# Kernel tuning notes

Hardware: AMD Instinct MI355X
Metric: run time of the kernel (lower is better)

Reference implementation:

```python
import jax, jax.numpy as jnp
import numpy as np

N_NODES = 50000
N_EDGES = 800000
IN_DIM = 128
HID = 128
OUT_DIM = 128
N_LAYERS = 6
NUM_GRAPHS = 128


def setup_inputs() -> dict:
    key = jax.random.key(0)
    ks = jax.random.split(key, 16)
    s = 0.05
    inp = {
        "x": jax.random.normal(ks[0], (N_NODES, IN_DIM), jnp.float32),
        "edge_index": jax.random.randint(ks[1], (2, N_EDGES), 0, N_NODES, jnp.int64 if jax.config.jax_enable_x64 else jnp.int32).astype(jnp.int32),
        "batch": jnp.sort(jax.random.randint(ks[2], (N_NODES,), 0, NUM_GRAPHS).astype(jnp.int32)),
        # pre linear
        "pre_w": jax.random.normal(ks[3], (IN_DIM, HID), jnp.float32) * s,
        "pre_b": jnp.zeros((HID,), jnp.float32),
        # GIN mlp per layer: Linear(H,H) -> ReLU -> Linear(H,H)
        "conv_w1": jax.random.normal(ks[4], (N_LAYERS, HID, HID), jnp.float32) * s,
        "conv_b1": jnp.zeros((N_LAYERS, HID), jnp.float32),
        "conv_w2": jax.random.normal(ks[5], (N_LAYERS, HID, HID), jnp.float32) * s,
        "conv_b2": jnp.zeros((N_LAYERS, HID), jnp.float32),
        # post MLP: Linear(7H, H) -> ReLU -> Linear(H, out)
        "post_w1": jax.random.normal(ks[6], (HID * (N_LAYERS + 1), HID), jnp.float32) * s,
        "post_b1": jnp.zeros((HID,), jnp.float32),
        "post_w2": jax.random.normal(ks[7], (HID, OUT_DIM), jnp.float32) * s,
        "post_b2": jnp.zeros((OUT_DIM,), jnp.float32),
    }
    return inp


def reference(x, edge_index, batch, pre_w, pre_b, conv_w1, conv_b1, conv_w2, conv_b2,
              post_w1, post_b1, post_w2, post_b2):
    src, dst = edge_index[0], edge_index[1]
    # pre linear
    h = x @ pre_w + pre_b  # [N, H]
    emb_list = [h]
    xres = h
    for i in range(N_LAYERS):
        # GINConv (eps=0): agg_j x_j over in-edges, then (1+eps)*x + agg -> MLP
        msg = h[src]  # [E, H] gather
        agg = jax.ops.segment_sum(msg, dst, num_segments=N_NODES)  # scatter-add
        z = h + agg
        z = jax.nn.relu(z @ conv_w1[i] + conv_b1[i]) @ conv_w2[i] + conv_b2[i]
        if i & 1:
            z = z + xres
            xres = z
        h = jax.nn.relu(z)
        emb_list.append(h)
    emb = jnp.concatenate(emb_list, axis=1)  # [N, (L+1)*H]
    # global add pool over graphs
    pooled = jax.ops.segment_sum(emb, batch, num_segments=NUM_GRAPHS)  # [G, (L+1)*H]
    out = jax.nn.relu(pooled @ post_w1 + post_b1) @ post_w2 + post_b2  # [G, OUT]
    return out
```

## Files before the change

kernel.cpp:

```cpp
#include <hip/hip_runtime.h>
#include <hip/hip_bf16.h>

#define HID 128

using bf16x8 = __attribute__((ext_vector_type(8))) short;
using f32x4  = __attribute__((ext_vector_type(4))) float;

__device__ inline float bf2f(unsigned int u16) {
    union { float f; unsigned int i; } v; v.i = u16 << 16; return v.f;
}
__device__ inline unsigned short f2bf(float f) {
    __hip_bfloat16 h = __float2bfloat16(f);
    return *reinterpret_cast<unsigned short*>(&h);
}


__global__ void zero_i32(int* __restrict__ p, int n) {
    int i = blockIdx.x * blockDim.x + threadIdx.x;
    if (i < n) p[i] = 0;
}

__global__ void count_deg(const int* __restrict__ dst, int* __restrict__ deg, int E) {
    int e = blockIdx.x * blockDim.x + threadIdx.x;
    if (e < E) atomicAdd(&deg[dst[e]], 1);
}

__global__ __launch_bounds__(256) void block_sums(const int* __restrict__ deg,
                                                  int* __restrict__ bsum, int n) {
    __shared__ int red[256];
    int t = threadIdx.x;
    int i = blockIdx.x * 256 + t;
    red[t] = (i < n) ? deg[i] : 0;
    __syncthreads();
    for (int off = 128; off > 0; off >>= 1) {
        if (t < off) red[t] += red[t + off];
        __syncthreads();
    }
    if (t == 0) bsum[blockIdx.x] = red[0];
}

__global__ __launch_bounds__(1024) void scan_bsums(const int* __restrict__ bsum,
                                                   int* __restrict__ bstart, int nb) {
    __shared__ int s[1024];
    int t = threadIdx.x;
    s[t] = (t < nb) ? bsum[t] : 0;
    __syncthreads();
    for (int off = 1; off < 1024; off <<= 1) {
        int v = (t >= off) ? s[t - off] : 0;
        __syncthreads();
        s[t] += v;
        __syncthreads();
    }
    if (t < nb) bstart[t] = (t == 0) ? 0 : s[t - 1];
}

__global__ __launch_bounds__(256) void scan_within(const int* __restrict__ deg,
                                                   const int* __restrict__ bstart,
                                                   int* __restrict__ row_ptr,
                                                   int* __restrict__ pos, int n) {
    __shared__ int s[256];
    int b = blockIdx.x, t = threadIdx.x;
    int i = b * 256 + t;
    int v = (i < n) ? deg[i] : 0;
    s[t] = v;
    __syncthreads();
    for (int off = 1; off < 256; off <<= 1) {
        int u = (t >= off) ? s[t - off] : 0;
        __syncthreads();
        s[t] += u;
        __syncthreads();
    }
    if (i < n) {
        int excl = bstart[b] + s[t] - v;
        row_ptr[i] = excl;
        pos[i] = excl;
        if (i == n - 1) row_ptr[n] = bstart[b] + s[t];
    }
}

__global__ void fill_csr(const int* __restrict__ src, const int* __restrict__ dst,
                         int* __restrict__ pos, int* __restrict__ csr_src, int E) {
    int e = blockIdx.x * blockDim.x + threadIdx.x;
    if (e < E) {
        int p = atomicAdd(&pos[dst[e]], 1);
        csr_src[p] = src[e];
    }
}

__global__ void graph_starts(const int* __restrict__ batch, int* __restrict__ gstart,
                             int n, int G) {
    int g = blockIdx.x * blockDim.x + threadIdx.x;
    if (g > G) return;
    int lo = 0, hi = n;
    while (lo < hi) { int m = (lo + hi) >> 1; if (batch[m] < g) lo = m + 1; else hi = m; }
    gstart[g] = lo;
}


__global__ void f32_to_bf16_vec(const float* __restrict__ in,
                                unsigned short* __restrict__ out, int n8) {
    int i = blockIdx.x * blockDim.x + threadIdx.x;
    if (i >= n8) return;
    const float4* in4 = (const float4*)in;
    float4 a = in4[i * 2], b = in4[i * 2 + 1];
    uint4 o;
    o.x = f2bf(a.x) | ((unsigned)f2bf(a.y) << 16);
    o.y = f2bf(a.z) | ((unsigned)f2bf(a.w) << 16);
    o.z = f2bf(b.x) | ((unsigned)f2bf(b.y) << 16);
    o.w = f2bf(b.z) | ((unsigned)f2bf(b.w) << 16);
    ((uint4*)out)[i] = o;
}

__global__ void transpose_kc(const float* __restrict__ W, unsigned short* __restrict__ Wt,
                             int K, int C, int total) {
    int tid = blockIdx.x * blockDim.x + threadIdx.x;
    if (tid >= total) return;
    int kc = K * C;
    int mat = tid / kc;
    int rem = tid - mat * kc;
    int c = rem / K;
    int k = rem - c * K;
    Wt[tid] = f2bf(W[(size_t)mat * kc + (size_t)k * C + c]);
}

template <bool ODD>
__global__ __launch_bounds__(128) void fused_layer(const unsigned short* __restrict__ emb,
                                                   int slice_u4, int row_u4,
                                                   const int* __restrict__ row_ptr,
                                                   const int* __restrict__ csr_src,
                                                   const unsigned short* __restrict__ Wt1,
                                                   const float* __restrict__ b1,
                                                   const unsigned short* __restrict__ Wt2,
                                                   const float* __restrict__ b2,
                                                   unsigned short* __restrict__ xres,
                                                   unsigned short* __restrict__ h_out,
                                                   int out_stride, int N) {
    __shared__ __align__(16) char zt[16 * 256];
    __shared__ __align__(16) char tt[16 * 256];
    int t = threadIdx.x;
    int rowbase = blockIdx.x * 16;

    {
        int nl = t >> 3;
        int lane8 = t & 7;
        int node = rowbase + nl;
        const uint4* h4 = (const uint4*)emb;
        float sa0=0,sa1=0,sa2=0,sa3=0,sa4=0,sa5=0,sa6=0,sa7=0;
        float sb0=0,sb1=0,sb2=0,sb3=0,sb4=0,sb5=0,sb6=0,sb7=0;
        if (node < N) {
            size_t base = (size_t)node * row_u4 + slice_u4;
            uint4 u0 = h4[base + lane8];
            uint4 u1 = h4[base + lane8 + 8];
            sa0 = bf2f(u0.x & 0xffff); sa1 = bf2f(u0.x >> 16);
            sa2 = bf2f(u0.y & 0xffff); sa3 = bf2f(u0.y >> 16);
            sa4 = bf2f(u0.z & 0xffff); sa5 = bf2f(u0.z >> 16);
            sa6 = bf2f(u0.w & 0xffff); sa7 = bf2f(u0.w >> 16);
            sb0 = bf2f(u1.x & 0xffff); sb1 = bf2f(u1.x >> 16);
            sb2 = bf2f(u1.y & 0xffff); sb3 = bf2f(u1.y >> 16);
            sb4 = bf2f(u1.z & 0xffff); sb5 = bf2f(u1.z >> 16);
            sb6 = bf2f(u1.w & 0xffff); sb7 = bf2f(u1.w >> 16);
            int e0 = row_ptr[node], e1 = row_ptr[node + 1];
            int e = e0;
            for (; e + 1 < e1; e += 2) {
                int n0 = csr_src[e], n1 = csr_src[e + 1];
                size_t p0 = (size_t)n0 * row_u4 + slice_u4;
                size_t p1 = (size_t)n1 * row_u4 + slice_u4;
                uint4 v0 = h4[p0 + lane8];
                uint4 v1 = h4[p0 + lane8 + 8];
                uint4 w0 = h4[p1 + lane8];
                uint4 w1 = h4[p1 + lane8 + 8];
                sa0 += bf2f(v0.x & 0xffff); sa1 += bf2f(v0.x >> 16);
                sa2 += bf2f(v0.y & 0xffff); sa3 += bf2f(v0.y >> 16);
                sa4 += bf2f(v0.z & 0xffff); sa5 += bf2f(v0.z >> 16);
                sa6 += bf2f(v0.w & 0xffff); sa7 += bf2f(v0.w >> 16);
                sb0 += bf2f(v1.x & 0xffff); sb1 += bf2f(v1.x >> 16);
                sb2 += bf2f(v1.y & 0xffff); sb3 += bf2f(v1.y >> 16);
                sb4 += bf2f(v1.z & 0xffff); sb5 += bf2f(v1.z >> 16);
                sb6 += bf2f(v1.w & 0xffff); sb7 += bf2f(v1.w >> 16);
                sa0 += bf2f(w0.x & 0xffff); sa1 += bf2f(w0.x >> 16);
                sa2 += bf2f(w0.y & 0xffff); sa3 += bf2f(w0.y >> 16);
                sa4 += bf2f(w0.z & 0xffff); sa5 += bf2f(w0.z >> 16);
                sa6 += bf2f(w0.w & 0xffff); sa7 += bf2f(w0.w >> 16);
                sb0 += bf2f(w1.x & 0xffff); sb1 += bf2f(w1.x >> 16);
                sb2 += bf2f(w1.y & 0xffff); sb3 += bf2f(w1.y >> 16);
                sb4 += bf2f(w1.z & 0xffff); sb5 += bf2f(w1.z >> 16);
                sb6 += bf2f(w1.w & 0xffff); sb7 += bf2f(w1.w >> 16);
            }
            if (e < e1) {
                size_t p0 = (size_t)csr_src[e] * row_u4 + slice_u4;
                uint4 v0 = h4[p0 + lane8];
                uint4 v1 = h4[p0 + lane8 + 8];
                sa0 += bf2f(v0.x & 0xffff); sa1 += bf2f(v0.x >> 16);
                sa2 += bf2f(v0.y & 0xffff); sa3 += bf2f(v0.y >> 16);
                sa4 += bf2f(v0.z & 0xffff); sa5 += bf2f(v0.z >> 16);
                sa6 += bf2f(v0.w & 0xffff); sa7 += bf2f(v0.w >> 16);
                sb0 += bf2f(v1.x & 0xffff); sb1 += bf2f(v1.x >> 16);
                sb2 += bf2f(v1.y & 0xffff); sb3 += bf2f(v1.y >> 16);
                sb4 += bf2f(v1.z & 0xffff); sb5 += bf2f(v1.z >> 16);
                sb6 += bf2f(v1.w & 0xffff); sb7 += bf2f(v1.w >> 16);
            }
        }
        uint4 oa, ob;
        oa.x = f2bf(sa0) | ((unsigned)f2bf(sa1) << 16);
        oa.y = f2bf(sa2) | ((unsigned)f2bf(sa3) << 16);
        oa.z = f2bf(sa4) | ((unsigned)f2bf(sa5) << 16);
        oa.w = f2bf(sa6) | ((unsigned)f2bf(sa7) << 16);
        ob.x = f2bf(sb0) | ((unsigned)f2bf(sb1) << 16);
        ob.y = f2bf(sb2) | ((unsigned)f2bf(sb3) << 16);
        ob.z = f2bf(sb4) | ((unsigned)f2bf(sb5) << 16);
        ob.w = f2bf(sb6) | ((unsigned)f2bf(sb7) << 16);
        int swz = (nl & 7) << 4;
        *(uint4*)(zt + nl * 256 + ((lane8 * 16) ^ swz)) = oa;
        *(uint4*)(zt + nl * 256 + (((lane8 + 8) * 16) ^ swz)) = ob;
    }
    __syncthreads();

    int wave = t >> 6, lane = t & 63, l15 = lane & 15, l4 = lane >> 4;
    int colbase = wave * 64;

    f32x4 acc[4];
#pragma unroll
    for (int ct = 0; ct < 4; ct++) acc[ct] = (f32x4){0.f, 0.f, 0.f, 0.f};

#pragma unroll
    for (int kk = 0; kk < 4; kk++) {
        int k0 = kk * 32 + l4 * 8;
        bf16x8 a0 = *(const bf16x8*)(zt + l15 * 256 + ((k0 * 2) ^ ((l15 & 7) << 4)));
#pragma unroll
        for (int ct = 0; ct < 4; ct++) {
            bf16x8 b = *(const bf16x8*)&Wt1[(size_t)(colbase + ct * 16 + l15) * HID + k0];
            acc[ct] = __builtin_amdgcn_mfma_f32_16x16x32_bf16(a0, b, acc[ct], 0, 0, 0);
        }
    }

#pragma unroll
    for (int ct = 0; ct < 4; ct++) {
        int col = colbase + ct * 16 + l15;
        float bc = b1[col];
#pragma unroll
        for (int j = 0; j < 4; j++) {
            int r = l4 * 4 + j;
            float v = fmaxf(acc[ct][j] + bc, 0.f);
            *(unsigned short*)(tt + r * 256 + ((col * 2) ^ ((r & 7) << 4))) = f2bf(v);
        }
    }
    __syncthreads();

#pragma unroll
    for (int ct = 0; ct < 4; ct++) acc[ct] = (f32x4){0.f, 0.f, 0.f, 0.f};
#pragma unroll
    for (int kk = 0; kk < 4; kk++) {
        int k0 = kk * 32 + l4 * 8;
        bf16x8 a0 = *(const bf16x8*)(tt + l15 * 256 + ((k0 * 2) ^ ((l15 & 7) << 4)));
#pragma unroll
        for (int ct = 0; ct < 4; ct++) {
            bf16x8 b = *(const bf16x8*)&Wt2[(size_t)(colbase + ct * 16 + l15) * HID + k0];
            acc[ct] = __builtin_amdgcn_mfma_f32_16x16x32_bf16(a0, b, acc[ct], 0, 0, 0);
        }
    }

#pragma unroll
    for (int ct = 0; ct < 4; ct++) {
        int col = colbase + ct * 16 + l15;
        float bc = b2[col];
#pragma unroll
        for (int j = 0; j < 4; j++) {
            int r = l4 * 4 + j;
            int rg = rowbase + r;
            if (rg < N) {
                float v = acc[ct][j] + bc;
                if (ODD) {
                    v += bf2f(xres[(size_t)rg * HID + col]);
                    xres[(size_t)rg * HID + col] = f2bf(v);
                }
                h_out[(size_t)rg * out_stride + col] = f2bf(fmaxf(v, 0.f));
            }
        }
    }
}

__global__ __launch_bounds__(256) void linear_pre(const unsigned short* __restrict__ in,
                                                  const unsigned short* __restrict__ Wt,
                                                  const float* __restrict__ bias,
                                                  unsigned short* __restrict__ out,
                                                  int out_stride,
                                                  unsigned short* __restrict__ pre_out, int M) {
    int tid = threadIdx.x;
    int wave = tid >> 6, lane = tid & 63;
    int l15 = lane & 15, l4 = lane >> 4;
    int rowbase = blockIdx.x * 64 + wave * 16;
    f32x4 acc[8];
#pragma unroll
    for (int ct = 0; ct < 8; ct++) acc[ct] = (f32x4){0.f, 0.f, 0.f, 0.f};
    int r0 = min(rowbase + l15, M - 1);
#pragma unroll
    for (int kk = 0; kk < 4; kk++) {
        int k0 = kk * 32 + l4 * 8;
        bf16x8 a0 = *(const bf16x8*)&in[(size_t)r0 * HID + k0];
#pragma unroll
        for (int ct = 0; ct < 8; ct++) {
            bf16x8 b = *(const bf16x8*)&Wt[(size_t)(ct * 16 + l15) * HID + k0];
            acc[ct] = __builtin_amdgcn_mfma_f32_16x16x32_bf16(a0, b, acc[ct], 0, 0, 0);
        }
    }
#pragma unroll
    for (int ct = 0; ct < 8; ct++) {
        int col = ct * 16 + l15;
        float bc = bias[col];
#pragma unroll
        for (int j = 0; j < 4; j++) {
            int r = rowbase + l4 * 4 + j;
            if (r < M) {
                float v = acc[ct][j] + bc;
                unsigned short bv = f2bf(v);
                pre_out[(size_t)r * HID + col] = bv;
                out[(size_t)r * out_stride + col] = bv;
            }
        }
    }
}

__global__ __launch_bounds__(128) void pool_all(const unsigned short* __restrict__ emb,
                                                const int* __restrict__ gstart,
                                                float* __restrict__ part, int EMB) {
    int g = blockIdx.x >> 3, sub = blockIdx.x & 7;
    int t = threadIdx.x;
    if (t >= 112) return;
    const uint4* e4 = (const uint4*)emb;
    int row_u4 = EMB / 8;
    int n0 = gstart[g], n1 = gstart[g + 1];
    float s[8] = {0.f, 0.f, 0.f, 0.f, 0.f, 0.f, 0.f, 0.f};
    for (int n = n0 + sub; n < n1; n += 8) {
        uint4 v = e4[(size_t)n * row_u4 + t];
        s[0] += bf2f(v.x & 0xffff); s[1] += bf2f(v.x >> 16);
        s[2] += bf2f(v.y & 0xffff); s[3] += bf2f(v.y >> 16);
        s[4] += bf2f(v.z & 0xffff); s[5] += bf2f(v.z >> 16);
        s[6] += bf2f(v.w & 0xffff); s[7] += bf2f(v.w >> 16);
    }
    float4* p4 = (float4*)&part[(size_t)blockIdx.x * EMB + t * 8];
    p4[0] = (float4){s[0], s[1], s[2], s[3]};
    p4[1] = (float4){s[4], s[5], s[6], s[7]};
}

__global__ __launch_bounds__(128) void pool_fin(const float* __restrict__ part,
                                                unsigned short* __restrict__ pooled,
                                                int EMB) {
    int idx = blockIdx.x * 128 + threadIdx.x;
    int g = idx / EMB, c = idx - g * EMB;
    float s = 0.f;
#pragma unroll
    for (int sub = 0; sub < 8; sub++)
        s += part[(size_t)(g * 8 + sub) * EMB + c];
    pooled[idx] = f2bf(s);
}

__global__ __launch_bounds__(256) void post_mfma(const unsigned short* __restrict__ pooled,
                                                 const unsigned short* __restrict__ w1t,
                                                 const float* __restrict__ b1,
                                                 const unsigned short* __restrict__ w2t,
                                                 const float* __restrict__ b2,
                                                 float* __restrict__ out, int EMB) {
    __shared__ __align__(16) char lds[128 * 256];
    int t = threadIdx.x;
    int wave = t >> 6, lane = t & 63, l15 = lane & 15, l4 = lane >> 4;
    int wrow = wave * 32;
    f32x4 acc[2][8];
#pragma unroll
    for (int rt = 0; rt < 2; rt++)
#pragma unroll
        for (int ct = 0; ct < 8; ct++) acc[rt][ct] = (f32x4){0.f, 0.f, 0.f, 0.f};
    int r0 = wrow + l15, r1 = r0 + 16;
#pragma unroll 4
    for (int kk = 0; kk < EMB / 32; kk++) {
        int k0 = kk * 32 + l4 * 8;
        bf16x8 a0 = *(const bf16x8*)&pooled[(size_t)r0 * EMB + k0];
        bf16x8 a1 = *(const bf16x8*)&pooled[(size_t)r1 * EMB + k0];
#pragma unroll
        for (int ct = 0; ct < 8; ct++) {
            bf16x8 b = *(const bf16x8*)&w1t[(size_t)(ct * 16 + l15) * EMB + k0];
            acc[0][ct] = __builtin_amdgcn_mfma_f32_16x16x32_bf16(a0, b, acc[0][ct], 0, 0, 0);
            acc[1][ct] = __builtin_amdgcn_mfma_f32_16x16x32_bf16(a1, b, acc[1][ct], 0, 0, 0);
        }
    }
#pragma unroll
    for (int ct = 0; ct < 8; ct++) {
        int col = ct * 16 + l15;
        float bc = b1[col];
#pragma unroll
        for (int rt = 0; rt < 2; rt++)
#pragma unroll
            for (int j = 0; j < 4; j++) {
                int r = wrow + rt * 16 + l4 * 4 + j;
                float v = fmaxf(acc[rt][ct][j] + bc, 0.f);
                *(unsigned short*)(lds + r * 256 + ((col * 2) ^ ((r & 7) << 4))) = f2bf(v);
            }
    }
    __syncthreads();
#pragma unroll
    for (int rt = 0; rt < 2; rt++)
#pragma unroll
        for (int ct = 0; ct < 8; ct++) acc[rt][ct] = (f32x4){0.f, 0.f, 0.f, 0.f};
#pragma unroll
    for (int kk = 0; kk < 4; kk++) {
        int k0 = kk * 32 + l4 * 8;
        bf16x8 a0 = *(const bf16x8*)(lds + r0 * 256 + ((k0 * 2) ^ ((r0 & 7) << 4)));
        bf16x8 a1 = *(const bf16x8*)(lds + r1 * 256 + ((k0 * 2) ^ ((r1 & 7) << 4)));
#pragma unroll
        for (int ct = 0; ct < 8; ct++) {
            bf16x8 b = *(const bf16x8*)&w2t[(size_t)(ct * 16 + l15) * HID + k0];
            acc[0][ct] = __builtin_amdgcn_mfma_f32_16x16x32_bf16(a0, b, acc[0][ct], 0, 0, 0);
            acc[1][ct] = __builtin_amdgcn_mfma_f32_16x16x32_bf16(a1, b, acc[1][ct], 0, 0, 0);
        }
    }
#pragma unroll
    for (int ct = 0; ct < 8; ct++) {
        int col = ct * 16 + l15;
        float bc = b2[col];
#pragma unroll
        for (int rt = 0; rt < 2; rt++)
#pragma unroll
            for (int j = 0; j < 4; j++) {
                int r = wrow + rt * 16 + l4 * 4 + j;
                out[(size_t)r * HID + col] = acc[rt][ct][j] + bc;
            }
    }
}


extern "C" void kernel_launch(void* const* d_in, const int* in_sizes, int n_in,
                              void* d_out, int out_size, void* d_ws, size_t ws_size,
                              hipStream_t stream) {
    const float* x       = (const float*)d_in[0];
    const int* edge_index= (const int*)d_in[1];
    const int* batch     = (const int*)d_in[2];
    const float* pre_w   = (const float*)d_in[3];
    const float* pre_b   = (const float*)d_in[4];
    const float* conv_w1 = (const float*)d_in[5];
    const float* conv_b1 = (const float*)d_in[6];
    const float* conv_w2 = (const float*)d_in[7];
    const float* conv_b2 = (const float*)d_in[8];
    const float* post_w1 = (const float*)d_in[9];
    const float* post_b1 = (const float*)d_in[10];
    const float* post_w2 = (const float*)d_in[11];
    const float* post_b2 = (const float*)d_in[12];
    float* outp = (float*)d_out;

    int N = in_sizes[0] / HID;
    int E = in_sizes[1] / 2;
    int L = in_sizes[5] / (HID * HID);
    int G = out_size / HID;
    int EMB = (L + 1) * HID;

    const int* src = edge_index;
    const int* dst = edge_index + E;

    char* w = (char*)d_ws;
    auto alloc = [&](size_t bytes) -> char* {
        char* p = w;
        w += (bytes + 255) & ~(size_t)255;
        return p;
    };
    unsigned short* emb   = (unsigned short*)alloc((size_t)N * EMB * 2);
    unsigned short* x_bf  = (unsigned short*)alloc((size_t)N * HID * 2);
    unsigned short* xres  = (unsigned short*)alloc((size_t)N * HID * 2);
    float* part   = (float*)alloc((size_t)G * 8 * EMB * 4);
    unsigned short* pooled = (unsigned short*)alloc((size_t)G * EMB * 2);
    unsigned short* Wt_pre = (unsigned short*)alloc((size_t)HID * HID * 2);
    unsigned short* Wt_c1  = (unsigned short*)alloc((size_t)L * HID * HID * 2);
    unsigned short* Wt_c2  = (unsigned short*)alloc((size_t)L * HID * HID * 2);
    unsigned short* w1t    = (unsigned short*)alloc((size_t)EMB * HID * 2);
    unsigned short* w2t    = (unsigned short*)alloc((size_t)HID * HID * 2);
    int* deg      = (int*)alloc((size_t)(N + 1) * 4);
    int* row_ptr  = (int*)alloc((size_t)(N + 1) * 4);
    int* pos      = (int*)alloc((size_t)(N + 1) * 4);
    int* bsum     = (int*)alloc((size_t)1024 * 4);
    int* bstart   = (int*)alloc((size_t)1024 * 4);
    int* csr_src  = (int*)alloc((size_t)E * 4);
    int* gstart   = (int*)alloc((size_t)(G + 1) * 4);
    (void)ws_size; (void)n_in;

    int eb = (E + 255) / 256;
    int nb = (N + 255) / 256;

    zero_i32<<<nb, 256, 0, stream>>>(deg, N);
    count_deg<<<eb, 256, 0, stream>>>(dst, deg, E);
    block_sums<<<nb, 256, 0, stream>>>(deg, bsum, N);
    scan_bsums<<<1, 1024, 0, stream>>>(bsum, bstart, nb);
    scan_within<<<nb, 256, 0, stream>>>(deg, bstart, row_ptr, pos, N);
    fill_csr<<<eb, 256, 0, stream>>>(src, dst, pos, csr_src, E);
    graph_starts<<<1, 256, 0, stream>>>(batch, gstart, N, G);

    f32_to_bf16_vec<<<(N * HID / 8 + 255) / 256, 256, 0, stream>>>(x, x_bf, N * HID / 8);
    transpose_kc<<<(HID * HID + 255) / 256, 256, 0, stream>>>(pre_w, Wt_pre, HID, HID, HID * HID);
    transpose_kc<<<(L * HID * HID + 255) / 256, 256, 0, stream>>>(conv_w1, Wt_c1, HID, HID, L * HID * HID);
    transpose_kc<<<(L * HID * HID + 255) / 256, 256, 0, stream>>>(conv_w2, Wt_c2, HID, HID, L * HID * HID);
    transpose_kc<<<(EMB * HID + 255) / 256, 256, 0, stream>>>(post_w1, w1t, EMB, HID, EMB * HID);
    transpose_kc<<<(HID * HID + 255) / 256, 256, 0, stream>>>(post_w2, w2t, HID, HID, HID * HID);

    int gb64 = (N + 63) / 64;
    int gb16 = (N + 15) / 16;

    linear_pre<<<gb64, 256, 0, stream>>>(x_bf, Wt_pre, pre_b, emb, EMB, xres, N);

    for (int i = 0; i < L; i++) {
        unsigned short* slice_out = emb + (size_t)(i + 1) * HID;
        if (i & 1) {
            fused_layer<true><<<gb16, 128, 0, stream>>>(
                emb, i * 16, EMB / 8, row_ptr, csr_src,
                Wt_c1 + (size_t)i * HID * HID, conv_b1 + i * HID,
                Wt_c2 + (size_t)i * HID * HID, conv_b2 + i * HID,
                xres, slice_out, EMB, N);
        } else {
            fused_layer<false><<<gb16, 128, 0, stream>>>(
                emb, i * 16, EMB / 8, row_ptr, csr_src,
                Wt_c1 + (size_t)i * HID * HID, conv_b1 + i * HID,
                Wt_c2 + (size_t)i * HID * HID, conv_b2 + i * HID,
                xres, slice_out, EMB, N);
        }
    }

    pool_all<<<G * 8, 128, 0, stream>>>(emb, gstart, part, EMB);
    pool_fin<<<(G * EMB) / 128, 128, 0, stream>>>(part, pooled, EMB);
    post_mfma<<<1, 256, 0, stream>>>(pooled, w1t, post_b1, w2t, post_b2, outp, EMB);
}
```

Baseline: 582.0 us.

## Split each node's neighbor gather across two lane groups with 256-thread blocks

Doubles the fused GIN layer block to 256 threads so each node's edge list is processed by two 8-lane subgroups taking alternating edges. The partial sums are combined with a cross-lane shuffle, and each subgroup writes one half of the row. The MFMA phase is redistributed so four waves each compute 32 output columns instead of two waves with 64. The aim is more memory-level parallelism in the latency-bound neighbor gather, at the cost of extra shuffles and possibly lower occupancy per block.

Result: faster. 524.5 us (-9.9%).

```diff
diff --git a/kernel.cpp b/kernel.cpp
--- a/kernel.cpp
+++ b/kernel.cpp
@@ -124,7 +124,7 @@
 }
 
 template <bool ODD>
-__global__ __launch_bounds__(128) void fused_layer(const unsigned short* __restrict__ emb,
+__global__ __launch_bounds__(256) void fused_layer(const unsigned short* __restrict__ emb,
                                                    int slice_u4, int row_u4,
                                                    const int* __restrict__ row_ptr,
                                                    const int* __restrict__ csr_src,
@@ -141,30 +141,33 @@
     int rowbase = blockIdx.x * 16;
 
     {
-        int nl = t >> 3;
+        int nl = t >> 4;
+        int sub = (t >> 3) & 1;
         int lane8 = t & 7;
         int node = rowbase + nl;
         const uint4* h4 = (const uint4*)emb;
         float sa0=0,sa1=0,sa2=0,sa3=0,sa4=0,sa5=0,sa6=0,sa7=0;
         float sb0=0,sb1=0,sb2=0,sb3=0,sb4=0,sb5=0,sb6=0,sb7=0;
         if (node < N) {
-            size_t base = (size_t)node * row_u4 + slice_u4;
-            uint4 u0 = h4[base + lane8];
-            uint4 u1 = h4[base + lane8 + 8];
-            sa0 = bf2f(u0.x & 0xffff); sa1 = bf2f(u0.x >> 16);
-            sa2 = bf2f(u0.y & 0xffff); sa3 = bf2f(u0.y >> 16);
-            sa4 = bf2f(u0.z & 0xffff); sa5 = bf2f(u0.z >> 16);
-            sa6 = bf2f(u0.w & 0xffff); sa7 = bf2f(u0.w >> 16);
-            sb0 = bf2f(u1.x & 0xffff); sb1 = bf2f(u1.x >> 16);
-            sb2 = bf2f(u1.y & 0xffff); sb3 = bf2f(u1.y >> 16);
-            sb4 = bf2f(u1.z & 0xffff); sb5 = bf2f(u1.z >> 16);
-            sb6 = bf2f(u1.w & 0xffff); sb7 = bf2f(u1.w >> 16);
+            if (sub == 0) {
+                size_t base = (size_t)node * row_u4 + slice_u4;
+                uint4 u0 = h4[base + lane8];
+                uint4 u1 = h4[base + lane8 + 8];
+                sa0 = bf2f(u0.x & 0xffff); sa1 = bf2f(u0.x >> 16);
+                sa2 = bf2f(u0.y & 0xffff); sa3 = bf2f(u0.y >> 16);
+                sa4 = bf2f(u0.z & 0xffff); sa5 = bf2f(u0.z >> 16);
+                sa6 = bf2f(u0.w & 0xffff); sa7 = bf2f(u0.w >> 16);
+                sb0 = bf2f(u1.x & 0xffff); sb1 = bf2f(u1.x >> 16);
+                sb2 = bf2f(u1.y & 0xffff); sb3 = bf2f(u1.y >> 16);
+                sb4 = bf2f(u1.z & 0xffff); sb5 = bf2f(u1.z >> 16);
+                sb6 = bf2f(u1.w & 0xffff); sb7 = bf2f(u1.w >> 16);
+            }
             int e0 = row_ptr[node], e1 = row_ptr[node + 1];
-            int e = e0;
-            for (; e + 1 < e1; e += 2) {
-                int n0 = csr_src[e], n1 = csr_src[e + 1];
-                size_t p0 = (size_t)n0 * row_u4 + slice_u4;
-                size_t p1 = (size_t)n1 * row_u4 + slice_u4;
+            int e = e0 + sub;
+            for (; e + 2 < e1; e += 4) {
+                int i0 = csr_src[e], i1 = csr_src[e + 2];
+                size_t p0 = (size_t)i0 * row_u4 + slice_u4;
+                size_t p1 = (size_t)i1 * row_u4 + slice_u4;
                 uint4 v0 = h4[p0 + lane8];
                 uint4 v1 = h4[p0 + lane8 + 8];
                 uint4 w0 = h4[p1 + lane8];
@@ -200,41 +203,51 @@
                 sb6 += bf2f(v1.w & 0xffff); sb7 += bf2f(v1.w >> 16);
             }
         }
-        uint4 oa, ob;
-        oa.x = f2bf(sa0) | ((unsigned)f2bf(sa1) << 16);
-        oa.y = f2bf(sa2) | ((unsigned)f2bf(sa3) << 16);
-        oa.z = f2bf(sa4) | ((unsigned)f2bf(sa5) << 16);
-        oa.w = f2bf(sa6) | ((unsigned)f2bf(sa7) << 16);
-        ob.x = f2bf(sb0) | ((unsigned)f2bf(sb1) << 16);
-        ob.y = f2bf(sb2) | ((unsigned)f2bf(sb3) << 16);
-        ob.z = f2bf(sb4) | ((unsigned)f2bf(sb5) << 16);
-        ob.w = f2bf(sb6) | ((unsigned)f2bf(sb7) << 16);
-        int swz = (nl & 7) << 4;
-        *(uint4*)(zt + nl * 256 + ((lane8 * 16) ^ swz)) = oa;
-        *(uint4*)(zt + nl * 256 + (((lane8 + 8) * 16) ^ swz)) = ob;
+        sa0 += __shfl_xor(sa0, 8); sa1 += __shfl_xor(sa1, 8);
+        sa2 += __shfl_xor(sa2, 8); sa3 += __shfl_xor(sa3, 8);
+        sa4 += __shfl_xor(sa4, 8); sa5 += __shfl_xor(sa5, 8);
+        sa6 += __shfl_xor(sa6, 8); sa7 += __shfl_xor(sa7, 8);
+        sb0 += __shfl_xor(sb0, 8); sb1 += __shfl_xor(sb1, 8);
+        sb2 += __shfl_xor(sb2, 8); sb3 += __shfl_xor(sb3, 8);
+        sb4 += __shfl_xor(sb4, 8); sb5 += __shfl_xor(sb5, 8);
+        sb6 += __shfl_xor(sb6, 8); sb7 += __shfl_xor(sb7, 8);
+        uint4 o;
+        if (sub == 0) {
+            o.x = f2bf(sa0) | ((unsigned)f2bf(sa1) << 16);
+            o.y = f2bf(sa2) | ((unsigned)f2bf(sa3) << 16);
+            o.z = f2bf(sa4) | ((unsigned)f2bf(sa5) << 16);
+            o.w = f2bf(sa6) | ((unsigned)f2bf(sa7) << 16);
+        } else {
+            o.x = f2bf(sb0) | ((unsigned)f2bf(sb1) << 16);
+            o.y = f2bf(sb2) | ((unsigned)f2bf(sb3) << 16);
+            o.z = f2bf(sb4) | ((unsigned)f2bf(sb5) << 16);
+            o.w = f2bf(sb6) | ((unsigned)f2bf(sb7) << 16);
+        }
+        int chunk = lane8 + sub * 8;
+        *(uint4*)(zt + nl * 256 + ((chunk * 16) ^ ((nl & 7) << 4))) = o;
     }
     __syncthreads();
 
     int wave = t >> 6, lane = t & 63, l15 = lane & 15, l4 = lane >> 4;
-    int colbase = wave * 64;
-
-    f32x4 acc[4];
-#pragma unroll
-    for (int ct = 0; ct < 4; ct++) acc[ct] = (f32x4){0.f, 0.f, 0.f, 0.f};
+    int colbase = wave * 32;
+
+    f32x4 acc[2];
+#pragma unroll
+    for (int ct = 0; ct < 2; ct++) acc[ct] = (f32x4){0.f, 0.f, 0.f, 0.f};
 
 #pragma unroll
     for (int kk = 0; kk < 4; kk++) {
         int k0 = kk * 32 + l4 * 8;
         bf16x8 a0 = *(const bf16x8*)(zt + l15 * 256 + ((k0 * 2) ^ ((l15 & 7) << 4)));
 #pragma unroll
-        for (int ct = 0; ct < 4; ct++) {
+        for (int ct = 0; ct < 2; ct++) {
             bf16x8 b = *(const bf16x8*)&Wt1[(size_t)(colbase + ct * 16 + l15) * HID + k0];
             acc[ct] = __builtin_amdgcn_mfma_f32_16x16x32_bf16(a0, b, acc[ct], 0, 0, 0);
         }
     }
 
 #pragma unroll
-    for (int ct = 0; ct < 4; ct++) {
+    for (int ct = 0; ct < 2; ct++) {
         int col = colbase + ct * 16 + l15;
         float bc = b1[col];
 #pragma unroll
@@ -247,20 +260,20 @@
     __syncthreads();
 
 #pragma unroll
-    for (int ct = 0; ct < 4; ct++) acc[ct] = (f32x4){0.f, 0.f, 0.f, 0.f};
+    for (int ct = 0; ct < 2; ct++) acc[ct] = (f32x4){0.f, 0.f, 0.f, 0.f};
 #pragma unroll
     for (int kk = 0; kk < 4; kk++) {
         int k0 = kk * 32 + l4 * 8;
         bf16x8 a0 = *(const bf16x8*)(tt + l15 * 256 + ((k0 * 2) ^ ((l15 & 7) << 4)));
 #pragma unroll
-        for (int ct = 0; ct < 4; ct++) {
+        for (int ct = 0; ct < 2; ct++) {
             bf16x8 b = *(const bf16x8*)&Wt2[(size_t)(colbase + ct * 16 + l15) * HID + k0];
             acc[ct] = __builtin_amdgcn_mfma_f32_16x16x32_bf16(a0, b, acc[ct], 0, 0, 0);
         }
     }
 
 #pragma unroll
-    for (int ct = 0; ct < 4; ct++) {
+    for (int ct = 0; ct < 2; ct++) {
         int col = colbase + ct * 16 + l15;
         float bc = b2[col];
 #pragma unroll
@@ -505,13 +518,13 @@
     for (int i = 0; i < L; i++) {
         unsigned short* slice_out = emb + (size_t)(i + 1) * HID;
         if (i & 1) {
-            fused_layer<true><<<gb16, 128, 0, stream>>>(
+            fused_layer<true><<<gb16, 256, 0, stream>>>(
                 emb, i * 16, EMB / 8, row_ptr, csr_src,
                 Wt_c1 + (size_t)i * HID * HID, conv_b1 + i * HID,
                 Wt_c2 + (size_t)i * HID * HID, conv_b2 + i * HID,
                 xres, slice_out, EMB, N);
         } else {
-            fused_layer<false><<<gb16, 128, 0, stream>>>(
+            fused_layer<false><<<gb16, 256, 0, stream>>>(
                 emb, i * 16, EMB / 8, row_ptr, csr_src,
                 Wt_c1 + (size_t)i * HID * HID, conv_b1 + i * HID,
                 Wt_c2 + (size_t)i * HID * HID, conv_b2 + i * HID,
```
